# Optimization experiments

Measured on AMD Instinct MI355X. Metric: run time of the kernel, lower is better.

The kernel has to match this reference:

```python
import jax, jax.numpy as jnp
import numpy as np
from jax import lax

B, L, D, F, K = 16, 1024, 384, 1536, 3
MAX_DUR = 10          # clamp on per-token duration (makes output length static)
T_OUT = L * MAX_DUR   # padded expanded length
ALPHA = 1.0
EPS = 1e-5


def conv1d_same(x_ncl, w, b):
    # x_ncl: [B, Cin, L], w: [Cout, Cin, K]
    y = lax.conv_general_dilated(x_ncl, w, window_strides=(1,), padding='SAME',
                                 dimension_numbers=('NCH', 'OIH', 'NCH'))
    return y + b[None, :, None]


def conv_block(x, wA, bA, wB, bB):
    # x: [B, L, D] -> Conv(D->F) ReLU Conv(F->D) ReLU -> [B, L, D]
    h = x.transpose(0, 2, 1)
    h = jax.nn.relu(conv1d_same(h, wA, bA))
    h = jax.nn.relu(conv1d_same(h, wB, bB))
    return h.transpose(0, 2, 1)


def layernorm(x, g, b):
    mu = jnp.mean(x, axis=-1, keepdims=True)
    var = jnp.var(x, axis=-1, keepdims=True)
    return (x - mu) * lax.rsqrt(var + EPS) * g + b


def setup_inputs() -> dict:
    key = jax.random.key(0)
    ks = jax.random.split(key, 8)
    s = 0.02
    return {
        'y': jax.random.normal(ks[0], (B, L, D), jnp.float32),
        'token_lengths': jax.random.randint(ks[1], (B,), 1, L + 1).astype(jnp.int32),
        'w1a': jax.random.normal(ks[2], (F, D, K), jnp.float32) * s,
        'b1a': jnp.zeros((F,), jnp.float32),
        'w1b': jax.random.normal(ks[3], (D, F, K), jnp.float32) * s,
        'b1b': jnp.zeros((D,), jnp.float32),
        'g1': jnp.ones((D,), jnp.float32),
        'be1': jnp.zeros((D,), jnp.float32),
        'w2a': jax.random.normal(ks[4], (F, D, K), jnp.float32) * s,
        'b2a': jnp.zeros((F,), jnp.float32),
        'w2b': jax.random.normal(ks[5], (D, F, K), jnp.float32) * s,
        'b2b': jnp.zeros((D,), jnp.float32),
        'g2': jnp.ones((D,), jnp.float32),
        'be2': jnp.zeros((D,), jnp.float32),
        'wl': jax.random.normal(ks[6], (D, 1), jnp.float32) * s,
        'bl': jnp.zeros((1,), jnp.float32),
    }


def reference(y, token_lengths, w1a, b1a, w1b, b1b, g1, be1,
              w2a, b2a, w2b, b2b, g2, be2, wl, bl):
    # DurationPredictor (eval mode: dropout is identity)
    h = conv_block(y, w1a, b1a, w1b, b1b)
    h = layernorm(h, g1, be1)
    h = conv_block(h, w2a, b2a, w2b, b2b)
    h = layernorm(h, g2, be2)
    preds = h @ wl + bl                      # [B, L, 1]

    # lengths = round(alpha * exp(preds)), masked to valid tokens, clamped
    lns = jnp.round(ALPHA * jnp.exp(preds[..., 0]))
    lns = jnp.clip(lns, 0, MAX_DUR).astype(jnp.int32)        # [B, L]
    mask = jnp.arange(L)[None, :] < token_lengths[:, None]
    lns = jnp.where(mask, lns, 0)

    # ragged repeat_interleave + pad, fully vectorized:
    # output frame t maps to token idx = searchsorted(cumsum(lns), t, 'right')
    csum = jnp.cumsum(lns, axis=1)                            # [B, L]
    totals = csum[:, -1]                                      # [B]
    t = jnp.arange(T_OUT, dtype=jnp.int32)
    idx = jax.vmap(lambda c: jnp.searchsorted(c, t, side='right'))(csum)  # [B, T_OUT]
    idx = jnp.minimum(idx, L - 1)
    gathered = jnp.take_along_axis(y, idx[..., None], axis=1)  # [B, T_OUT, D]
    valid = t[None, :] < totals[:, None]
    enlarged = jnp.where(valid[..., None], gathered, 0.0)
    return enlarged, totals
```

## Files before the change

### kernel.cpp

```cpp
#include <hip/hip_runtime.h>
#include <hip/hip_bf16.h>

#define BB 16
#define LL 1024
#define DD 384
#define FF 1536
#define KK 3
#define T_OUT 10240
#define MAX_DUR 10

#define PADL 1026
#define LO_SCALE 2048.0f
#define LO_INV   4.8828125e-4f

typedef _Float16 f16x8 __attribute__((ext_vector_type(8)));
typedef float    f32x4 __attribute__((ext_vector_type(4)));

__device__ __forceinline__ void gll16(const void* g, void* l) {
    __builtin_amdgcn_global_load_lds(
        (const __attribute__((address_space(1))) void*)g,
        (__attribute__((address_space(3))) void*)l, 16, 0, 0);
}

__device__ __forceinline__ void split_write(float v, _Float16* hi, _Float16* lo, size_t off) {
    _Float16 h = (_Float16)v;
    hi[off] = h;
    lo[off] = (_Float16)((v - (float)h) * LO_SCALE);
}

__device__ __forceinline__ float split_read(const _Float16* hi, const _Float16* lo, size_t off) {
    return (float)hi[off] + (float)lo[off] * LO_INV;
}

__global__ void wfrag_k(const float* __restrict__ w, _Float16* __restrict__ hi,
                        _Float16* __restrict__ lo, int O, int I) {
    int id = blockIdx.x * 256 + threadIdx.x;
    int total = O * 3 * I;
    if (id >= total) return;
    int e = id & 7;
    int lane = (id >> 3) & 63;
    int rest = id >> 9;
    int nKT = (3 * I) >> 5;
    int ktl = rest % nKT;
    int ot = rest / nKT;
    int o = ot * 16 + (lane & 15);
    int koff = ((lane >> 4) << 3) + e;
    int kseg = ktl % 3;
    int i = (ktl / 3) * 32 + koff;
    float v = w[(o * I + i) * 3 + kseg];
    split_write(v, hi, lo, id);
}

__global__ void ysplit_k(const float* __restrict__ y, _Float16* __restrict__ hi,
                         _Float16* __restrict__ lo) {
    int id = blockIdx.x * 256 + threadIdx.x;
    if (id >= BB * PADL * DD) return;
    int d = id % DD;
    int r = id / DD;
    int b = r / PADL;
    int lr = r - b * PADL;
    float v = 0.f;
    if (lr >= 1 && lr <= LL) v = y[((size_t)(b << 10) + (lr - 1)) * DD + d];
    split_write(v, hi, lo, id);
}

__global__ void padzero_k(_Float16* __restrict__ hi, _Float16* __restrict__ lo, int width) {
    int id = blockIdx.x * 256 + threadIdx.x;
    if (id >= BB * 2 * width) return;
    int b = id / (2 * width);
    int rem = id - b * 2 * width;
    int row = (rem / width) ? (PADL - 1) : 0;
    int c = rem % width;
    size_t off = (size_t)(b * PADL + row) * width + c;
    hi[off] = (_Float16)0.f;
    lo[off] = (_Float16)0.f;
}

template<int CIN, int COUT, int KTOT, int NN>
__global__ __launch_bounds__(256, 3) void gemm_breg(
        const _Float16* __restrict__ Ahi, const _Float16* __restrict__ Alo,
        const _Float16* __restrict__ WfH, const _Float16* __restrict__ WfL,
        const float* __restrict__ bias,
        _Float16* __restrict__ Ohi, _Float16* __restrict__ Olo) {
    constexpr int BM   = 128;
    constexpr int AC   = (BM + 2) * 4;
    constexpr int AC4  = AC / 4;
    constexpr int AIT  = (AC4 + 63) / 64;
    constexpr int AHH  = AC * 8;
    constexpr int nKT  = KTOT >> 5;
    constexpr int nJ   = nKT / 3;
    __shared__ __align__(16) _Float16 lds_h[4 * AHH];
    const int tid = threadIdx.x;
    const int lane = tid & 63;
    const int w = tid >> 6;
    const int lm = lane & 15, lq = lane >> 4;
    const int xcd = blockIdx.x & 7;
    const int t2 = blockIdx.x >> 3;
    const int g  = t2 / (4 * NN);
    const int r  = t2 - g * (4 * NN);
    const int n_t = r >> 2;
    const int mi  = r & 3;
    const int m_t = ((g * 4 + mi) << 3) + xcd;
    const int m0 = m_t * BM;
    const int n0 = n_t * 64;
    const int b = m0 >> 10;
    const int l0 = m0 & 1023;
    const int rowBase = b * PADL + l0;
    const int wm = (w >> 1) * 64, wn = (w & 1) * 32;

    f32x4 accM[4][2], accC[4][2];
    const f32x4 zz = {0.f, 0.f, 0.f, 0.f};
    #pragma unroll
    for (int i = 0; i < 4; ++i)
        #pragma unroll
        for (int jj = 0; jj < 2; ++jj) { accM[i][jj] = zz; accC[i][jj] = zz; }

    int aRowK[AIT];
    bool aAct[AIT];
    #pragma unroll
    for (int it = 0; it < AIT; ++it) {
        int cl = it * 64 + lane;
        int s  = w * AC4 + cl;
        int p = s >> 3, sl = s & 7;
        int t = sl ^ (p & 7);
        int m = p * 2 + (t >> 2);
        int k8 = t & 3;
        aRowK[it] = (rowBase + m) * CIN + k8 * 8;
        aAct[it] = (cl < AC4);
    }
    int baseB[2];
    #pragma unroll
    for (int jj = 0; jj < 2; ++jj) {
        int ntg = (n0 >> 4) + (w & 1) * 2 + jj;
        baseB[jj] = (ntg * nKT * 64 + lane) * 8;
    }
    int aOff[12];
    #pragma unroll
    for (int t = 0; t < 12; ++t) {
        int row = wm + (t & 3) * 16 + lm + (t >> 2);
        int p = row >> 1;
        int sl = (((row & 1) << 2) | lq) ^ (p & 7);
        aOff[t] = p * 64 + sl * 8;
    }

    auto stageA = [&](int jt, int bidx) {
        int d0 = jt << 5;
        _Float16* abase = lds_h + bidx * (2 * AHH);
        #pragma unroll
        for (int it = 0; it < AIT; ++it) {
            size_t aoff = (size_t)(unsigned)(aRowK[it] + d0);
            _Float16* hb = abase + (w * AC4 + it * 64) * 8;
            if (aAct[it]) {
                gll16(Ahi + aoff, hb);
                gll16(Alo + aoff, hb + AHH);
            }
        }
    };

    auto loadB = [&](int p, f16x8* dH, f16x8* dL) {
        int pc = p < nKT ? p : nKT - 1;
        #pragma unroll
        for (int jj = 0; jj < 2; ++jj) {
            size_t off = (size_t)(unsigned)(baseB[jj] + pc * 512);
            dH[jj] = *(const f16x8*)(WfH + off);
            dL[jj] = *(const f16x8*)(WfL + off);
        }
    };

    auto compute = [&](const _Float16* ab, int s, const f16x8* bh, const f16x8* bl) {
        __builtin_amdgcn_s_setprio(1);
        #pragma unroll
        for (int i = 0; i < 4; ++i) {
            int off = aOff[s * 4 + i];
            f16x8 aH = *(const f16x8*)(ab + off);
            f16x8 aL = *(const f16x8*)(ab + AHH + off);
            #pragma unroll
            for (int jj = 0; jj < 2; ++jj) {
                accM[i][jj] = __builtin_amdgcn_mfma_f32_16x16x32_f16(aH, bh[jj], accM[i][jj], 0, 0, 0);
                accC[i][jj] = __builtin_amdgcn_mfma_f32_16x16x32_f16(aH, bl[jj], accC[i][jj], 0, 0, 0);
                accC[i][jj] = __builtin_amdgcn_mfma_f32_16x16x32_f16(aL, bh[jj], accC[i][jj], 0, 0, 0);
            }
        }
        __builtin_amdgcn_s_setprio(0);
    };

    f16x8 b0H[2], b0L[2], b1H[2], b1L[2];
    stageA(0, 0);
    __builtin_amdgcn_sched_barrier(0);
    loadB(0, b0H, b0L);
    __builtin_amdgcn_sched_barrier(0);
    asm volatile("s_waitcnt vmcnt(4)" ::: "memory");
    __builtin_amdgcn_s_barrier();

    for (int jm = 0; jm < nJ; jm += 2) {
        const _Float16* bufE = lds_h;
        const _Float16* bufO = lds_h + 2 * AHH;
        const int p0 = 3 * jm;
        loadB(p0 + 1, b1H, b1L);
        stageA(jm + 1 < nJ ? jm + 1 : nJ - 1, 1);
        __builtin_amdgcn_sched_barrier(0);
        asm volatile("s_waitcnt vmcnt(10)" ::: "memory");
        __builtin_amdgcn_sched_barrier(0);
        compute(bufE, 0, b0H, b0L);
        __builtin_amdgcn_sched_barrier(0);

        loadB(p0 + 2, b0H, b0L);
        __builtin_amdgcn_sched_barrier(0);
        asm volatile("s_waitcnt vmcnt(10)" ::: "memory");
        __builtin_amdgcn_sched_barrier(0);
        compute(bufE, 1, b1H, b1L);
        __builtin_amdgcn_sched_barrier(0);

        loadB(p0 + 3, b1H, b1L);
        __builtin_amdgcn_sched_barrier(0);
        asm volatile("s_waitcnt vmcnt(4)" ::: "memory");
        __builtin_amdgcn_sched_barrier(0);
        compute(bufE, 2, b0H, b0L);
        __builtin_amdgcn_sched_barrier(0);
        __builtin_amdgcn_s_barrier();
        loadB(p0 + 4, b0H, b0L);
        stageA(jm + 2 < nJ ? jm + 2 : nJ - 1, 0);
        __builtin_amdgcn_sched_barrier(0);
        asm volatile("s_waitcnt vmcnt(10)" ::: "memory");
        __builtin_amdgcn_sched_barrier(0);
        compute(bufO, 0, b1H, b1L);
        __builtin_amdgcn_sched_barrier(0);

        loadB(p0 + 5, b1H, b1L);
        __builtin_amdgcn_sched_barrier(0);
        asm volatile("s_waitcnt vmcnt(10)" ::: "memory");
        __builtin_amdgcn_sched_barrier(0);
        compute(bufO, 1, b0H, b0L);
        __builtin_amdgcn_sched_barrier(0);

        loadB(p0 + 6, b0H, b0L);
        __builtin_amdgcn_sched_barrier(0);
        asm volatile("s_waitcnt vmcnt(4)" ::: "memory");
        __builtin_amdgcn_sched_barrier(0);
        compute(bufO, 2, b1H, b1L);
        __builtin_amdgcn_sched_barrier(0);
        __builtin_amdgcn_s_barrier();
    }
    #pragma unroll
    for (int i = 0; i < 4; ++i)
        #pragma unroll
        for (int jj = 0; jj < 2; ++jj) {
            int n_g = n0 + wn + jj * 16 + lm;
            float bv = bias[n_g];
            #pragma unroll
            for (int rr = 0; rr < 4; ++rr) {
                int l = l0 + wm + i * 16 + lq * 4 + rr;
                float v = accM[i][jj][rr] + accC[i][jj][rr] * LO_INV + bv;
                v = fmaxf(v, 0.f);
                size_t off = (size_t)(b * PADL + 1 + l) * COUT + n_g;
                split_write(v, Ohi, Olo, off);
            }
        }
}

__global__ __launch_bounds__(128) void ln_split_k(
        _Float16* __restrict__ hi, _Float16* __restrict__ lo,
        const float* __restrict__ g, const float* __restrict__ be) {
    const int row = blockIdx.x;
    const int b = row >> 10, l = row & 1023;
    const size_t base = (size_t)(b * PADL + 1 + l) * DD;
    const int tid = threadIdx.x;
    float v0 = split_read(hi, lo, base + tid);
    float v1 = split_read(hi, lo, base + tid + 128);
    float v2 = split_read(hi, lo, base + tid + 256);

    __shared__ float sh[2];
    float s = v0 + v1 + v2;
    #pragma unroll
    for (int o = 32; o > 0; o >>= 1) s += __shfl_down(s, o, 64);
    if ((tid & 63) == 0) sh[tid >> 6] = s;
    __syncthreads();
    float mu = (sh[0] + sh[1]) * (1.f / DD);
    __syncthreads();
    float d0 = v0 - mu, d1 = v1 - mu, d2 = v2 - mu;
    float q = d0 * d0 + d1 * d1 + d2 * d2;
    #pragma unroll
    for (int o = 32; o > 0; o >>= 1) q += __shfl_down(q, o, 64);
    if ((tid & 63) == 0) sh[tid >> 6] = q;
    __syncthreads();
    float var = (sh[0] + sh[1]) * (1.f / DD);
    float rs = rsqrtf(var + 1e-5f);
    split_write(d0 * rs * g[tid] + be[tid], hi, lo, base + tid);
    split_write(d1 * rs * g[tid + 128] + be[tid + 128], hi, lo, base + tid + 128);
    split_write(d2 * rs * g[tid + 256] + be[tid + 256], hi, lo, base + tid + 256);
}

__global__ __launch_bounds__(128) void ln_pred_split_k(
        const _Float16* __restrict__ hi, const _Float16* __restrict__ lo,
        const float* __restrict__ g, const float* __restrict__ be,
        const float* __restrict__ wl, const float* __restrict__ bl,
        const int* __restrict__ token_lengths, int* __restrict__ lns) {
    const int row = blockIdx.x;
    const int b = row >> 10, l = row & 1023;
    const size_t base = (size_t)(b * PADL + 1 + l) * DD;
    const int tid = threadIdx.x;
    float v0 = split_read(hi, lo, base + tid);
    float v1 = split_read(hi, lo, base + tid + 128);
    float v2 = split_read(hi, lo, base + tid + 256);

    __shared__ float sh[2];
    float s = v0 + v1 + v2;
    #pragma unroll
    for (int o = 32; o > 0; o >>= 1) s += __shfl_down(s, o, 64);
    if ((tid & 63) == 0) sh[tid >> 6] = s;
    __syncthreads();
    float mu = (sh[0] + sh[1]) * (1.f / DD);
    __syncthreads();
    float d0 = v0 - mu, d1 = v1 - mu, d2 = v2 - mu;
    float q = d0 * d0 + d1 * d1 + d2 * d2;
    #pragma unroll
    for (int o = 32; o > 0; o >>= 1) q += __shfl_down(q, o, 64);
    if ((tid & 63) == 0) sh[tid >> 6] = q;
    __syncthreads();
    float var = (sh[0] + sh[1]) * (1.f / DD);
    float rs = rsqrtf(var + 1e-5f);
    __syncthreads();
    float p = (d0 * rs * g[tid]       + be[tid])       * wl[tid]
            + (d1 * rs * g[tid + 128] + be[tid + 128]) * wl[tid + 128]
            + (d2 * rs * g[tid + 256] + be[tid + 256]) * wl[tid + 256];
    #pragma unroll
    for (int o = 32; o > 0; o >>= 1) p += __shfl_down(p, o, 64);
    if ((tid & 63) == 0) sh[tid >> 6] = p;
    __syncthreads();
    if (tid == 0) {
        float pred = sh[0] + sh[1] + bl[0];
        float e = expf(pred);
        float r = rintf(e);
        r = fminf(fmaxf(r, 0.f), (float)MAX_DUR);
        int v = (int)r;
        if (l >= token_lengths[b]) v = 0;
        lns[row] = v;
    }
}

__global__ __launch_bounds__(1024) void cumsum_k(
        const int* __restrict__ lns, int* __restrict__ csum,
        float* __restrict__ totals_out) {
    __shared__ int s[1024];
    const int b = blockIdx.x, tid = threadIdx.x;
    s[tid] = lns[(b << 10) + tid];
    __syncthreads();
    #pragma unroll
    for (int o = 1; o < 1024; o <<= 1) {
        int t = (tid >= o) ? s[tid - o] : 0;
        __syncthreads();
        s[tid] += t;
        __syncthreads();
    }
    csum[(b << 10) + tid] = s[tid];
    if (tid == 1023) totals_out[b] = (float)s[1023];
}

__global__ __launch_bounds__(256) void gather_k(
        const float* __restrict__ y, const int* __restrict__ csum,
        float* __restrict__ out) {
    int gid = blockIdx.x * 256 + threadIdx.x;
    int c4 = gid % 96;
    int rest = gid / 96;
    int t = rest % T_OUT;
    int b = rest / T_OUT;
    const int* c = csum + (b << 10);
    int total = c[1023];
    float4 r = make_float4(0.f, 0.f, 0.f, 0.f);
    if (t < total) {
        int lo = 0, hi = 1024;
        while (lo < hi) {
            int mid = (lo + hi) >> 1;
            if (c[mid] <= t) lo = mid + 1; else hi = mid;
        }
        int idx = min(lo, LL - 1);
        r = *(const float4*)(y + ((size_t)((b << 10) + idx)) * DD + (c4 << 2));
    }
    *(float4*)(out + ((size_t)b * T_OUT + t) * DD + (c4 << 2)) = r;
}

extern "C" void kernel_launch(void* const* d_in, const int* in_sizes, int n_in,
                              void* d_out, int out_size, void* d_ws, size_t ws_size,
                              hipStream_t stream) {
    const float* y   = (const float*)d_in[0];
    const int*   tok = (const int*)d_in[1];
    const float* w1a = (const float*)d_in[2];
    const float* b1a = (const float*)d_in[3];
    const float* w1b = (const float*)d_in[4];
    const float* b1b = (const float*)d_in[5];
    const float* g1  = (const float*)d_in[6];
    const float* be1 = (const float*)d_in[7];
    const float* w2a = (const float*)d_in[8];
    const float* b2a = (const float*)d_in[9];
    const float* w2b = (const float*)d_in[10];
    const float* b2b = (const float*)d_in[11];
    const float* g2  = (const float*)d_in[12];
    const float* be2 = (const float*)d_in[13];
    const float* wl  = (const float*)d_in[14];
    const float* bl  = (const float*)d_in[15];

    float* out = (float*)d_out;

    const size_t WN   = (size_t)FF * DD * KK;
    const size_t SN   = (size_t)BB * PADL * DD;
    const size_t H1N  = (size_t)BB * PADL * FF;
    _Float16* p = (_Float16*)d_ws;
    _Float16* Wh1a = p;              _Float16* Wl1a = Wh1a + WN;
    _Float16* Wh1b = Wl1a + WN;      _Float16* Wl1b = Wh1b + WN;
    _Float16* Wh2a = Wl1b + WN;      _Float16* Wl2a = Wh2a + WN;
    _Float16* Wh2b = Wl2a + WN;      _Float16* Wl2b = Wh2b + WN;
    _Float16* Shi  = Wl2b + WN;      _Float16* Slo  = Shi + SN;
    _Float16* H1hi = Slo + SN;       _Float16* H1lo = H1hi + H1N;
    int* lns  = (int*)(H1lo + H1N);
    int* csum = lns + BB * LL;

    const int M = BB * LL;

    {
        int n = FF * DD * KK;
        wfrag_k<<<(n + 255) / 256, 256, 0, stream>>>(w1a, Wh1a, Wl1a, FF, DD);
        wfrag_k<<<(n + 255) / 256, 256, 0, stream>>>(w1b, Wh1b, Wl1b, DD, FF);
        wfrag_k<<<(n + 255) / 256, 256, 0, stream>>>(w2a, Wh2a, Wl2a, FF, DD);
        wfrag_k<<<(n + 255) / 256, 256, 0, stream>>>(w2b, Wh2b, Wl2b, DD, FF);
        int ny = BB * PADL * DD;
        ysplit_k<<<(ny + 255) / 256, 256, 0, stream>>>(y, Shi, Slo);
        int np = BB * 2 * FF;
        padzero_k<<<(np + 255) / 256, 256, 0, stream>>>(H1hi, H1lo, FF);
    }
    gemm_breg<DD, FF, 3 * DD, FF / 64>
        <<<(FF / 64) * (M / 128), 256, 0, stream>>>(Shi, Slo, Wh1a, Wl1a, b1a, H1hi, H1lo);
    gemm_breg<FF, DD, 3 * FF, DD / 64>
        <<<(DD / 64) * (M / 128), 256, 0, stream>>>(H1hi, H1lo, Wh1b, Wl1b, b1b, Shi, Slo);
    ln_split_k<<<M, 128, 0, stream>>>(Shi, Slo, g1, be1);
    gemm_breg<DD, FF, 3 * DD, FF / 64>
        <<<(FF / 64) * (M / 128), 256, 0, stream>>>(Shi, Slo, Wh2a, Wl2a, b2a, H1hi, H1lo);
    gemm_breg<FF, DD, 3 * FF, DD / 64>
        <<<(DD / 64) * (M / 128), 256, 0, stream>>>(H1hi, H1lo, Wh2b, Wl2b, b2b, Shi, Slo);
    ln_pred_split_k<<<M, 128, 0, stream>>>(Shi, Slo, g2, be2, wl, bl, tok, lns);
    cumsum_k<<<BB, 1024, 0, stream>>>(lns, csum, out + (size_t)BB * T_OUT * DD);
    {
        long long n = (long long)BB * T_OUT * 96;
        gather_k<<<(int)((n + 255) / 256), 256, 0, stream>>>(y, csum, out);
    }
}
```

Baseline: 983.6 us.

## Use 128x128 tiles with 32x32x16 MFMA for the D-to-F conv GEMMs

Adds a gemm_big kernel that computes 128x128 output tiles using 32x32x16 f16 MFMA instructions, with a matching weight-fragment packing kernel (wfrag32_k). The two D->F expansion convolutions now use it instead of the 128x64 tile kernel. The goal is more reuse of each A tile loaded into LDS per block and fewer, larger MFMA issues. In exchange each thread holds more accumulator registers and occupancy drops to 2 blocks per CU, and the B-prefetch pipeline is shallower than the hand-tuned original.

```diff
diff --git a/kernel.cpp b/kernel.cpp
--- a/kernel.cpp
+++ b/kernel.cpp
@@ -15,6 +15,7 @@
 
 typedef _Float16 f16x8 __attribute__((ext_vector_type(8)));
 typedef float    f32x4 __attribute__((ext_vector_type(4)));
+typedef float    f32x16 __attribute__((ext_vector_type(16)));
 
 __device__ __forceinline__ void gll16(const void* g, void* l) {
     __builtin_amdgcn_global_load_lds(
@@ -51,6 +52,26 @@
     split_write(v, hi, lo, id);
 }
 
+__global__ void wfrag32_k(const float* __restrict__ w, _Float16* __restrict__ hi,
+                          _Float16* __restrict__ lo, int O, int I) {
+    int id = blockIdx.x * 256 + threadIdx.x;
+    int total = O * 3 * I;
+    if (id >= total) return;
+    int e = id & 7;
+    int lane = (id >> 3) & 63;
+    int ks = (id >> 9) & 1;
+    int rest = id >> 10;
+    int nKT = (3 * I) >> 5;
+    int ktl = rest % nKT;
+    int ot = rest / nKT;
+    int o = ot * 32 + (lane & 31);
+    int kseg = ktl % 3;
+    int kloc = ks * 16 + ((lane >> 5) << 3) + e;
+    int i = (ktl / 3) * 32 + kloc;
+    float v = w[(o * I + i) * 3 + kseg];
+    split_write(v, hi, lo, id);
+}
+
 __global__ void ysplit_k(const float* __restrict__ y, _Float16* __restrict__ hi,
                          _Float16* __restrict__ lo) {
     int id = blockIdx.x * 256 + threadIdx.x;
@@ -74,6 +95,191 @@
     size_t off = (size_t)(b * PADL + row) * width + c;
     hi[off] = (_Float16)0.f;
     lo[off] = (_Float16)0.f;
+}
+
+template<int CIN, int COUT, int KTOT, int NN>
+__global__ __launch_bounds__(256, 2) void gemm_big(
+        const _Float16* __restrict__ Ahi, const _Float16* __restrict__ Alo,
+        const _Float16* __restrict__ WfH, const _Float16* __restrict__ WfL,
+        const float* __restrict__ bias,
+        _Float16* __restrict__ Ohi, _Float16* __restrict__ Olo) {
+    constexpr int BM   = 128;
+    constexpr int AC   = (BM + 2) * 4;
+    constexpr int AC4  = AC / 4;
+    constexpr int AIT  = (AC4 + 63) / 64;
+    constexpr int AHH  = AC * 8;
+    constexpr int nKT  = KTOT >> 5;
+    constexpr int nJ   = nKT / 3;
+    __shared__ __align__(16) _Float16 lds_h[4 * AHH];
+    const int tid = threadIdx.x;
+    const int lane = tid & 63;
+    const int w = tid >> 6;
+    const int wr = w >> 1, wc = w & 1;
+    const int xcd = blockIdx.x & 7;
+    const int t2 = blockIdx.x >> 3;
+    const int g  = t2 / (4 * NN);
+    const int r  = t2 - g * (4 * NN);
+    const int n_t = r >> 2;
+    const int mi  = r & 3;
+    const int m_t = ((g * 4 + mi) << 3) + xcd;
+    const int m0 = m_t * BM;
+    const int n0 = n_t * 128;
+    const int b = m0 >> 10;
+    const int l0 = m0 & 1023;
+    const int rowBase = b * PADL + l0;
+
+    f32x16 accM[2][2], accC[2][2];
+    #pragma unroll
+    for (int mt = 0; mt < 2; ++mt)
+        #pragma unroll
+        for (int nt = 0; nt < 2; ++nt) {
+            #pragma unroll
+            for (int q = 0; q < 16; ++q) { accM[mt][nt][q] = 0.f; accC[mt][nt][q] = 0.f; }
+        }
+
+    int aRowK[AIT];
+    bool aAct[AIT];
+    #pragma unroll
+    for (int it = 0; it < AIT; ++it) {
+        int cl = it * 64 + lane;
+        int s  = w * AC4 + cl;
+        int p = s >> 3, sl = s & 7;
+        int t = sl ^ (p & 7);
+        int m = p * 2 + (t >> 2);
+        int k8 = t & 3;
+        aRowK[it] = (rowBase + m) * CIN + k8 * 8;
+        aAct[it] = (cl < AC4);
+    }
+    int bBase[2];
+    #pragma unroll
+    for (int nt = 0; nt < 2; ++nt) {
+        int ntg = (n0 >> 5) + wc * 2 + nt;
+        bBase[nt] = ntg * nKT * 1024 + lane * 8;
+    }
+    int aOffT[3][2][2];
+    #pragma unroll
+    for (int kseg = 0; kseg < 3; ++kseg)
+        #pragma unroll
+        for (int ks = 0; ks < 2; ++ks)
+            #pragma unroll
+            for (int mt = 0; mt < 2; ++mt) {
+                int row = wr * 64 + mt * 32 + (lane & 31) + kseg;
+                int k8 = ks * 2 + (lane >> 5);
+                int p_ = row >> 1;
+                int sl = (((row & 1) << 2) | k8) ^ (p_ & 7);
+                aOffT[kseg][ks][mt] = (p_ * 8 + sl) * 8;
+            }
+
+    auto stageA = [&](int jt, int bidx) {
+        int d0 = jt << 5;
+        _Float16* abase = lds_h + bidx * (2 * AHH);
+        #pragma unroll
+        for (int it = 0; it < AIT; ++it) {
+            size_t aoff = (size_t)(unsigned)(aRowK[it] + d0);
+            _Float16* hb = abase + (w * AC4 + it * 64) * 8;
+            if (aAct[it]) {
+                gll16(Ahi + aoff, hb);
+                gll16(Alo + aoff, hb + AHH);
+            }
+        }
+    };
+
+    f16x8 b0H[2], b0L[2], b1H[2], b1L[2];
+    auto loadBks0 = [&](int ktl) {
+        int kc = ktl < nKT ? ktl : nKT - 1;
+        #pragma unroll
+        for (int nt = 0; nt < 2; ++nt) {
+            size_t off = (size_t)(unsigned)(bBase[nt] + kc * 1024);
+            b0H[nt] = *(const f16x8*)(WfH + off);
+            b0L[nt] = *(const f16x8*)(WfL + off);
+        }
+    };
+    auto loadBks1 = [&](int ktl) {
+        int kc = ktl < nKT ? ktl : nKT - 1;
+        #pragma unroll
+        for (int nt = 0; nt < 2; ++nt) {
+            size_t off = (size_t)(unsigned)(bBase[nt] + kc * 1024 + 512);
+            b1H[nt] = *(const f16x8*)(WfH + off);
+            b1L[nt] = *(const f16x8*)(WfL + off);
+        }
+    };
+
+    auto phase = [&](const _Float16* ab, int ktl, int kseg) {
+        f16x8 aH[2], aL[2];
+        #pragma unroll
+        for (int mt = 0; mt < 2; ++mt) {
+            int off = aOffT[kseg][0][mt];
+            aH[mt] = *(const f16x8*)(ab + off);
+            aL[mt] = *(const f16x8*)(ab + AHH + off);
+        }
+        __builtin_amdgcn_s_setprio(1);
+        #pragma unroll
+        for (int mt = 0; mt < 2; ++mt)
+            #pragma unroll
+            for (int nt = 0; nt < 2; ++nt) {
+                accM[mt][nt] = __builtin_amdgcn_mfma_f32_32x32x16_f16(aH[mt], b0H[nt], accM[mt][nt], 0, 0, 0);
+                accC[mt][nt] = __builtin_amdgcn_mfma_f32_32x32x16_f16(aH[mt], b0L[nt], accC[mt][nt], 0, 0, 0);
+                accC[mt][nt] = __builtin_amdgcn_mfma_f32_32x32x16_f16(aL[mt], b0H[nt], accC[mt][nt], 0, 0, 0);
+            }
+        __builtin_amdgcn_s_setprio(0);
+        loadBks0(ktl + 1);
+        #pragma unroll
+        for (int mt = 0; mt < 2; ++mt) {
+            int off = aOffT[kseg][1][mt];
+            aH[mt] = *(const f16x8*)(ab + off);
+            aL[mt] = *(const f16x8*)(ab + AHH + off);
+        }
+        __builtin_amdgcn_s_setprio(1);
+        #pragma unroll
+        for (int mt = 0; mt < 2; ++mt)
+            #pragma unroll
+            for (int nt = 0; nt < 2; ++nt) {
+                accM[mt][nt] = __builtin_amdgcn_mfma_f32_32x32x16_f16(aH[mt], b1H[nt], accM[mt][nt], 0, 0, 0);
+                accC[mt][nt] = __builtin_amdgcn_mfma_f32_32x32x16_f16(aH[mt], b1L[nt], accC[mt][nt], 0, 0, 0);
+                accC[mt][nt] = __builtin_amdgcn_mfma_f32_32x32x16_f16(aL[mt], b1H[nt], accC[mt][nt], 0, 0, 0);
+            }
+        __builtin_amdgcn_s_setprio(0);
+        loadBks1(ktl + 1);
+    };
+
+    stageA(0, 0);
+    __builtin_amdgcn_sched_barrier(0);
+    loadBks0(0);
+    loadBks1(0);
+    __builtin_amdgcn_sched_barrier(0);
+    asm volatile("s_waitcnt vmcnt(8)" ::: "memory");
+    __builtin_amdgcn_s_barrier();
+    __builtin_amdgcn_sched_barrier(0);
+
+    for (int j = 0; j < nJ; ++j) {
+        const _Float16* ab = lds_h + (j & 1) * (2 * AHH);
+        const int p0 = 3 * j;
+        phase(ab, p0, 0);
+        stageA(j + 1 < nJ ? j + 1 : nJ - 1, (j + 1) & 1);
+        phase(ab, p0 + 1, 1);
+        phase(ab, p0 + 2, 2);
+        __builtin_amdgcn_sched_barrier(0);
+        asm volatile("s_waitcnt vmcnt(8)" ::: "memory");
+        __builtin_amdgcn_s_barrier();
+        __builtin_amdgcn_sched_barrier(0);
+    }
+    #pragma unroll
+    for (int nt = 0; nt < 2; ++nt) {
+        int n_g = n0 + wc * 64 + nt * 32 + (lane & 31);
+        float bv = bias[n_g];
+        #pragma unroll
+        for (int mt = 0; mt < 2; ++mt) {
+            #pragma unroll
+            for (int q = 0; q < 16; ++q) {
+                int rloc = (q & 3) + 8 * (q >> 2) + 4 * (lane >> 5);
+                int l = l0 + wr * 64 + mt * 32 + rloc;
+                float v = accM[mt][nt][q] + accC[mt][nt][q] * LO_INV + bv;
+                v = fmaxf(v, 0.f);
+                size_t off = (size_t)(b * PADL + 1 + l) * COUT + n_g;
+                split_write(v, Ohi, Olo, off);
+            }
+        }
+    }
 }
 
 template<int CIN, int COUT, int KTOT, int NN>
@@ -218,6 +424,7 @@
         compute(bufE, 2, b0H, b0L);
         __builtin_amdgcn_sched_barrier(0);
         __builtin_amdgcn_s_barrier();
+
         loadB(p0 + 4, b0H, b0L);
         stageA(jm + 2 < nJ ? jm + 2 : nJ - 1, 0);
         __builtin_amdgcn_sched_barrier(0);
@@ -418,22 +625,22 @@
 
     {
         int n = FF * DD * KK;
-        wfrag_k<<<(n + 255) / 256, 256, 0, stream>>>(w1a, Wh1a, Wl1a, FF, DD);
+        wfrag32_k<<<(n + 255) / 256, 256, 0, stream>>>(w1a, Wh1a, Wl1a, FF, DD);
         wfrag_k<<<(n + 255) / 256, 256, 0, stream>>>(w1b, Wh1b, Wl1b, DD, FF);
-        wfrag_k<<<(n + 255) / 256, 256, 0, stream>>>(w2a, Wh2a, Wl2a, FF, DD);
+        wfrag32_k<<<(n + 255) / 256, 256, 0, stream>>>(w2a, Wh2a, Wl2a, FF, DD);
         wfrag_k<<<(n + 255) / 256, 256, 0, stream>>>(w2b, Wh2b, Wl2b, DD, FF);
         int ny = BB * PADL * DD;
         ysplit_k<<<(ny + 255) / 256, 256, 0, stream>>>(y, Shi, Slo);
         int np = BB * 2 * FF;
         padzero_k<<<(np + 255) / 256, 256, 0, stream>>>(H1hi, H1lo, FF);
     }
-    gemm_breg<DD, FF, 3 * DD, FF / 64>
-        <<<(FF / 64) * (M / 128), 256, 0, stream>>>(Shi, Slo, Wh1a, Wl1a, b1a, H1hi, H1lo);
+    gemm_big<DD, FF, 3 * DD, FF / 128>
+        <<<(FF / 128) * (M / 128), 256, 0, stream>>>(Shi, Slo, Wh1a, Wl1a, b1a, H1hi, H1lo);
     gemm_breg<FF, DD, 3 * FF, DD / 64>
         <<<(DD / 64) * (M / 128), 256, 0, stream>>>(H1hi, H1lo, Wh1b, Wl1b, b1b, Shi, Slo);
     ln_split_k<<<M, 128, 0, stream>>>(Shi, Slo, g1, be1);
-    gemm_breg<DD, FF, 3 * DD, FF / 64>
-        <<<(FF / 64) * (M / 128), 256, 0, stream>>>(Shi, Slo, Wh2a, Wl2a, b2a, H1hi, H1lo);
+    gemm_big<DD, FF, 3 * DD, FF / 128>
+        <<<(FF / 128) * (M / 128), 256, 0, stream>>>(Shi, Slo, Wh2a, Wl2a, b2a, H1hi, H1lo);
     gemm_breg<FF, DD, 3 * FF, DD / 64>
         <<<(DD / 64) * (M / 128), 256, 0, stream>>>(H1hi, H1lo, Wh2b, Wl2b, b2b, Shi, Slo);
     ln_pred_split_k<<<M, 128, 0, stream>>>(Shi, Slo, g2, be2, wl, bl, tok, lns);
```

Result: no change. 996.9 us (+1.3%).
